# Kernel optimization log

Hardware: AMD Instinct MI355X
Metric: run time of the kernel (lower is better)

Reference implementation:

```python
import jax, jax.numpy as jnp
import numpy as np


def setup_inputs() -> dict:
    key = jax.random.key(0)
    ks = jax.random.split(key, 6)
    B, N, Cd, Qd, E, G = 256, 196, 2048, 1024, 1024, 8
    s = lambda d: 1.0 / np.sqrt(d)
    return {
        "context": jax.random.normal(ks[0], (B, N, Cd), dtype=jnp.float32),
        "query": jax.random.normal(ks[1], (B, Qd), dtype=jnp.float32),
        "Wq": jax.random.normal(ks[2], (E, Qd), dtype=jnp.float32) * s(Qd),
        "bq": jnp.zeros((E,), dtype=jnp.float32),
        "Wc": jax.random.normal(ks[3], (E, Cd), dtype=jnp.float32) * s(Cd),
        "bc": jnp.zeros((E,), dtype=jnp.float32),
        "Wo": jax.random.normal(ks[4], (G, E), dtype=jnp.float32) * s(E),
        "bo": jnp.zeros((G,), dtype=jnp.float32),
    }


def reference(context, query, Wq, bq, Wc, bc, Wo, bo):
    # query: [B, Qd] -> [B, 1, E]; context: [B, N, Cd] -> [B, N, E]
    qp = (query @ Wq.T + bq)[:, None, :]
    cp = jnp.einsum('bnc,ec->bne', context, Wc) + bc
    # dropout in eval mode (identity)
    combined = jnp.tanh(qp + cp)                      # [B, N, E]
    attn = jnp.einsum('bne,ge->bng', combined, Wo) + bo  # [B, N, G]
    weights = jax.nn.softmax(attn, axis=1)            # softmax over regions
    glimpses = jnp.einsum('bng,bnc->bgc', weights, context)  # [B, G, Cd]
    return glimpses.reshape(context.shape[0], -1)     # [B, G*Cd]
```

## Files before the change

kernel.cpp:

```cpp
#include <hip/hip_runtime.h>
#include <stdint.h>

typedef unsigned int u32;
typedef __bf16 bf16_t;
typedef bf16_t bf16x8 __attribute__((ext_vector_type(8)));
typedef bf16_t bf16x4 __attribute__((ext_vector_type(4)));
typedef float  f32x4  __attribute__((ext_vector_type(4)));

#define NB   256
#define NN   196
#define CD   2048
#define QD   1024
#define NE   1024
#define NG   8

#define WS_QP    0
#define WS_ATTN  (NB*NE*4)
#define WS_WCB   (WS_ATTN + NB*NG*NN*4)
#define WS_CTXB  (WS_WCB + (size_t)NE*CD*2)
#define WS_NEED  (WS_CTXB + (size_t)NB*NN*CD*2)

__device__ __forceinline__ bf16_t f2bf(float f){
  u32 u = __float_as_uint(f);
  u += 0x7fffu + ((u >> 16) & 1u);
  unsigned short h = (unsigned short)(u >> 16);
  return __builtin_bit_cast(bf16_t, h);
}

__device__ __forceinline__ float fast_tanh(float x){
  float e = __expf(2.0f * x);
  return 1.0f - 2.0f / (e + 1.0f);
}

__device__ __forceinline__ void load_lds16(const void* g, void* l){
  __builtin_amdgcn_global_load_lds(
      (const __attribute__((address_space(1))) void*)g,
      (__attribute__((address_space(3))) void*)l, 16, 0, 0);
}

__global__ __launch_bounds__(256)
void k_conv(const float* __restrict__ src, bf16_t* __restrict__ dst){
  size_t i = ((size_t)blockIdx.x * 256 + threadIdx.x) * 4;
  float4 v = *(const float4*)(src + i);
  bf16x4 o = { f2bf(v.x), f2bf(v.y), f2bf(v.z), f2bf(v.w) };
  *(bf16x4*)(dst + i) = o;
}

__global__ __launch_bounds__(256)
void k_convctx(const float* __restrict__ src, bf16_t* __restrict__ dst){
  size_t i = ((size_t)blockIdx.x * 256 + threadIdx.x) * 8;
  float4 a = *(const float4*)(src + i);
  float4 b = *(const float4*)(src + i + 4);
  bf16x8 o = { f2bf(a.x), f2bf(a.y), f2bf(a.z), f2bf(a.w),
               f2bf(b.x), f2bf(b.y), f2bf(b.z), f2bf(b.w) };
  *(bf16x8*)(dst + i) = o;
}

__global__ __launch_bounds__(256)
void k_qp(const float* __restrict__ query, const float* __restrict__ Wq,
          const float* __restrict__ bq, float* __restrict__ qp){
  __shared__ float qs[32][36];
  __shared__ float wsm[32][36];
  const u32 t  = threadIdx.x;
  const u32 e0 = blockIdx.x * 32, b0 = blockIdx.y * 32;
  const u32 r  = t >> 3, ci = (t & 7) * 4;
  const u32 tm = (t >> 4) * 2, tn = (t & 15) * 2;
  float c00 = 0.f, c01 = 0.f, c10 = 0.f, c11 = 0.f;
  for (u32 k0 = 0; k0 < QD; k0 += 32){
    float4 qv = *(const float4*)(query + (size_t)(b0 + r) * QD + k0 + ci);
    float4 wv = *(const float4*)(Wq    + (size_t)(e0 + r) * QD + k0 + ci);
    __syncthreads();
    *(float4*)&qs[r][ci]  = qv;
    *(float4*)&wsm[r][ci] = wv;
    __syncthreads();
    #pragma unroll
    for (int kq = 0; kq < 8; kq++){
      float4 a0 = *(const float4*)&qs[tm][kq*4];
      float4 a1 = *(const float4*)&qs[tm+1][kq*4];
      float4 b0v = *(const float4*)&wsm[tn][kq*4];
      float4 b1v = *(const float4*)&wsm[tn+1][kq*4];
      c00 += a0.x*b0v.x + a0.y*b0v.y + a0.z*b0v.z + a0.w*b0v.w;
      c01 += a0.x*b1v.x + a0.y*b1v.y + a0.z*b1v.z + a0.w*b1v.w;
      c10 += a1.x*b0v.x + a1.y*b0v.y + a1.z*b0v.z + a1.w*b0v.w;
      c11 += a1.x*b1v.x + a1.y*b1v.y + a1.z*b1v.z + a1.w*b1v.w;
    }
  }
  float bq0 = bq[e0+tn], bq1 = bq[e0+tn+1];
  qp[(size_t)(b0+tm  )*NE + e0+tn  ] = c00 + bq0;
  qp[(size_t)(b0+tm  )*NE + e0+tn+1] = c01 + bq1;
  qp[(size_t)(b0+tm+1)*NE + e0+tn  ] = c10 + bq0;
  qp[(size_t)(b0+tm+1)*NE + e0+tn+1] = c11 + bq1;
}

#define NKT 32

__global__ __launch_bounds__(512, 2)
void k_main8(const bf16_t* __restrict__ ctxb, const bf16_t* __restrict__ wcb,
             const float* __restrict__ qp, const float* __restrict__ bcv,
             const float* __restrict__ Wo, float* __restrict__ attn)
{
  __shared__ char smem[135168] __attribute__((aligned(128)));

  const u32 tid  = threadIdx.x;
  const u32 lane = tid & 63;
  const u32 w    = tid >> 6;
  const u32 q    = lane >> 4;
  const u32 r15  = lane & 15;
  const u32 x7   = r15 & 7;

  u32 d  = blockIdx.x;
  u32 wg = (d & 7) * 98u + (d >> 3);
  const u32 ms = wg >> 2;
  const u32 ec = wg & 3;
  const u32 m0 = ms * 256;
  const u32 e0 = ec * 256;

  const u32 srow = w*8 + (lane>>3);
  const u32 scol = ((lane&7) ^ ((lane>>3)&7)) * 8;
  const u32 sdst = w*1024u + lane*16u;

  const u32 arow = (w>>1)*32 + r15;
  const u32 brow = (w&1)*64 + r15;

  f32x4 acc[2][2][8];
  #pragma unroll
  for (int a1 = 0; a1 < 2; a1++)
    #pragma unroll
    for (int a2 = 0; a2 < 2; a2++)
      #pragma unroll
      for (int a3 = 0; a3 < 8; a3++) acc[a1][a2][a3] = (f32x4){0.f,0.f,0.f,0.f};

  auto stage = [&](u32 H){
    u32 tile = H >> 2;
    u32 half = H & 3;
    u32 kt   = tile < NKT ? tile : (NKT - 1);
    u32 buf  = tile & 1;
    u32 isb  = half >> 1;
    u32 hh   = half & 1;
    const bf16_t* src = (isb ? (wcb + (size_t)e0 * CD) : (ctxb + (size_t)m0 * CD))
                        + (size_t)(hh*128u + srow) * CD + kt*64u + scol;
    char* dst = smem + buf*65536u + isb*32768u + hh*16384u + sdst;
    load_lds16(src,                  dst);
    load_lds16(src + (size_t)64*CD,  dst + 8192);
  };

  stage(0); stage(1); stage(2); stage(3); stage(4);
  asm volatile("s_waitcnt vmcnt(4)" ::: "memory");
  __builtin_amdgcn_s_barrier();

#define PHASE(QM, QN, HOFF, DOVM) do {                                          \
    const char* Ab_ = smem + bufc*65536u;                                        \
    const char* Bb_ = Ab_ + 32768u;                                              \
    bf16x8 af[2][2], bq_[4][2];                                                  \
    _Pragma("unroll")                                                            \
    for (int m2 = 0; m2 < 2; m2++)                                               \
      _Pragma("unroll")                                                          \
      for (int kk = 0; kk < 2; kk++)                                             \
        af[m2][kk] = *(const bf16x8*)(Ab_ + ((QM)*128u + arow + m2*16u)*128u     \
                                          + (((u32)(kk*4) + q) ^ x7)*16u);       \
    _Pragma("unroll")                                                            \
    for (int nt = 0; nt < 4; nt++)                                               \
      _Pragma("unroll")                                                          \
      for (int kk = 0; kk < 2; kk++)                                             \
        bq_[nt][kk] = *(const bf16x8*)(Bb_ + ((QN)*128u + brow + nt*16u)*128u    \
                                           + (((u32)(kk*4) + q) ^ x7)*16u);      \
    stage(hbase + (HOFF));                                                       \
    __builtin_amdgcn_s_barrier();                                                \
    __builtin_amdgcn_s_setprio(1);                                               \
    _Pragma("unroll")                                                            \
    for (int m2 = 0; m2 < 2; m2++)                                               \
      _Pragma("unroll")                                                          \
      for (int nt = 0; nt < 4; nt++)                                             \
        _Pragma("unroll")                                                        \
        for (int kk = 0; kk < 2; kk++)                                           \
          acc[QM][QN][m2*4+nt] = __builtin_amdgcn_mfma_f32_16x16x32_bf16(        \
              af[m2][kk], bq_[nt][kk], acc[QM][QN][m2*4+nt], 0, 0, 0);           \
    __builtin_amdgcn_s_setprio(0);                                               \
    if (DOVM) asm volatile("s_waitcnt vmcnt(4)" ::: "memory");                   \
    __builtin_amdgcn_s_barrier();                                                \
  } while (0)

  for (u32 kt = 0; kt < NKT; kt++){
    const u32 bufc  = kt & 1;
    const u32 hbase = 4*kt + 5;
    PHASE(0, 0, 0, 1);
    PHASE(0, 1, 1, 0);
    PHASE(1, 0, 2, 0);
    PHASE(1, 1, 3, 1);
  }
#undef PHASE

  asm volatile("s_waitcnt vmcnt(0)" ::: "memory");
  __syncthreads();

  float*  qps  = (float*)(smem + 131072);
  float*  bcs  = (float*)(smem + 134144);
  const u32 b0   = m0 / 196u;
  const u32 bnd1 = (b0 + 1) * 196u - m0;
  const u32 bnd2 = bnd1 + 196u;

  for (u32 idx = tid; idx < 768; idx += 512){
    u32 bb = b0 + idx / 256u;
    if (bb > NB - 1) bb = NB - 1;
    qps[idx] = qp[(size_t)bb * NE + e0 + (idx & 255u)];
  }
  if (tid < 256) bcs[tid] = bcv[e0 + tid];

  bf16x8 wf[8];
  {
    u32 g = r15;
    #pragma unroll
    for (int kk = 0; kk < 8; kk++){
      #pragma unroll
      for (int rr = 0; rr < 8; rr++){
        u32 ei = e0 + kk*32 + q*8 + rr;
        float v = (g < NG) ? Wo[(size_t)g * NE + ei] : 0.0f;
        wf[kk][rr] = f2bf(v);
      }
    }
  }
  __syncthreads();

  #pragma unroll
  for (int qm = 0; qm < 2; qm++)
    #pragma unroll
    for (int qn = 0; qn < 2; qn++)
      #pragma unroll
      for (int t = 0; t < 8; t++){
        u32 rowb = qm*128u + (w>>1)*32u + (t>>2)*16u + q*4u;
        u32 col  = qn*128u + (w&1)*64u + (t&3)*16u + r15;
        float qb = bcs[col];
        #pragma unroll
        for (int r = 0; r < 4; r++){
          u32 row = rowb + r;
          u32 bidx = (row >= bnd1 ? 1u : 0u) + (row >= bnd2 ? 1u : 0u);
          float v = fast_tanh(acc[qm][qn][t][r] + qps[bidx*256u + col] + qb);
          u32 phys = (col >> 3) ^ (row & 7);
          *(bf16_t*)(smem + row*512u + phys*16u + (col&7)*2u) = f2bf(v);
        }
      }
  __syncthreads();

  #pragma unroll
  for (int i = 0; i < 2; i++){
    u32 nrow = w*32u + i*16u + r15;
    f32x4 at = (f32x4){0.f,0.f,0.f,0.f};
    #pragma unroll
    for (int kk = 0; kk < 8; kk++){
      u32 phys = ((u32)(kk*4) + q) ^ (nrow & 7);
      bf16x8 cf = *(const bf16x8*)(smem + nrow*512u + phys*16u);
      at = __builtin_amdgcn_mfma_f32_16x16x32_bf16(wf[kk], cf, at, 0, 0, 0);
    }
    if (q < 2){
      u32 mrow = m0 + nrow;
      u32 bb = mrow / 196u;
      u32 nn = mrow - bb * 196u;
      #pragma unroll
      for (int r = 0; r < 4; r++){
        u32 g = q*4 + r;
        atomicAdd(&attn[((size_t)bb * NG + g) * NN + nn], at[r]);
      }
    }
  }
}

#define BM 128
#define BN 128
#define BK 32
#define KSTEPS (CD/BK)

__global__ __launch_bounds__(256, 2)
void k_main_slow(const float* __restrict__ ctx, const bf16_t* __restrict__ wcb,
                 const float* __restrict__ qp, const float* __restrict__ bcv,
                 const float* __restrict__ Wo, float* __restrict__ attn)
{
  __shared__ char smem[40960] __attribute__((aligned(16)));
  const u32 tid  = threadIdx.x;
  const u32 lane = tid & 63;
  const u32 wave = tid >> 6;
  const u32 wm   = wave >> 1;
  const u32 wn   = wave & 1;
  u32 d  = blockIdx.x;
  u32 x  = d & 7;
  u32 s  = d >> 3;
  u32 ec = s & 7;
  u32 j  = s >> 3;
  u32 ms = j * 8 + x;
  const u32 m0 = ms * BM;
  const u32 e0 = ec * BN;
  const u32 ar  = tid >> 3;
  const u32 ac  = (tid & 7) * 4;
  const u32 br  = tid >> 2;
  const u32 bc8 = (tid & 3) * 8;
  const float*  actx = ctx + (size_t)m0 * CD;
  const bf16_t* bwc  = wcb + (size_t)e0 * CD;
  float4 av[4];
  uint4  bv[2];
  f32x4 acc[4][4];
  #pragma unroll
  for (int i = 0; i < 4; i++)
    #pragma unroll
    for (int jn = 0; jn < 4; jn++) acc[i][jn] = (f32x4){0.f,0.f,0.f,0.f};
  auto issue = [&](u32 ks){
    const u32 k0 = ks * BK;
    #pragma unroll
    for (int p = 0; p < 4; p++)
      av[p] = *(const float4*)(actx + (size_t)(ar + p*32) * CD + k0 + ac);
    #pragma unroll
    for (int p = 0; p < 2; p++)
      bv[p] = *(const uint4*)(bwc + (size_t)(br + p*64) * CD + k0 + bc8);
  };
  auto writebuf = [&](u32 buf){
    bf16_t* A  = (bf16_t*)(smem + buf * 10240u);
    bf16_t* Bb = (bf16_t*)(smem + 20480u + buf * 10240u);
    #pragma unroll
    for (int p = 0; p < 4; p++){
      bf16x4 o = { f2bf(av[p].x), f2bf(av[p].y), f2bf(av[p].z), f2bf(av[p].w) };
      *(bf16x4*)&A[(ar + p*32)*40 + ac] = o;
    }
    #pragma unroll
    for (int p = 0; p < 2; p++)
      *(uint4*)&Bb[(br + p*64)*40 + bc8] = bv[p];
  };
  auto compute = [&](u32 buf){
    bf16_t* A  = (bf16_t*)(smem + buf * 10240u);
    bf16_t* Bb = (bf16_t*)(smem + 20480u + buf * 10240u);
    const u32 kb = (lane >> 4) * 8;
    const u32 rm = wm*64 + (lane & 15);
    const u32 rn = wn*64 + (lane & 15);
    bf16x8 af[4], bfr[4];
    #pragma unroll
    for (int mt = 0; mt < 4; mt++) af[mt]  = *(const bf16x8*)&A[(rm + mt*16)*40 + kb];
    #pragma unroll
    for (int nt = 0; nt < 4; nt++) bfr[nt] = *(const bf16x8*)&Bb[(rn + nt*16)*40 + kb];
    #pragma unroll
    for (int mt = 0; mt < 4; mt++)
      #pragma unroll
      for (int nt = 0; nt < 4; nt++)
        acc[mt][nt] = __builtin_amdgcn_mfma_f32_16x16x32_bf16(af[mt], bfr[nt], acc[mt][nt], 0, 0, 0);
  };
  issue(0); writebuf(0);
  __syncthreads();
  for (u32 ks = 0; ks < KSTEPS; ks++){
    if (ks + 1 < KSTEPS) issue(ks + 1);
    compute(ks & 1);
    __syncthreads();
    if (ks + 1 < KSTEPS){
      writebuf((ks + 1) & 1);
      __syncthreads();
    }
  }
  float*  qp0  = (float*)(smem + 35840);
  float*  qp1  = (float*)(smem + 36352);
  float*  bcs  = (float*)(smem + 36864);
  bf16_t* comb = (bf16_t*)smem;
  const u32 b0  = m0 / 196u;
  const u32 bnd = (b0 + 1) * 196u - m0;
  if (tid < 128){
    qp0[tid] = qp[(size_t)b0 * NE + e0 + tid];
    bcs[tid] = bcv[e0 + tid];
  } else {
    u32 b1 = b0 + 1; if (b1 >= NB) b1 = NB - 1;
    qp1[tid - 128] = qp[(size_t)b1 * NE + e0 + (tid - 128)];
  }
  bf16x8 wf[4];
  {
    u32 g = lane & 15;
    #pragma unroll
    for (int kk = 0; kk < 4; kk++){
      #pragma unroll
      for (int rr = 0; rr < 8; rr++){
        u32 ei = e0 + kk*32 + (lane >> 4)*8 + rr;
        float v = (g < NG) ? Wo[(size_t)g * NE + ei] : 0.0f;
        wf[kk][rr] = f2bf(v);
      }
    }
  }
  __syncthreads();
  #pragma unroll
  for (int nt = 0; nt < 4; nt++){
    u32 el = wn*64 + nt*16 + (lane & 15);
    float qa = qp0[el];
    float qb = qp1[el];
    float bcx = bcs[el];
    #pragma unroll
    for (int mt = 0; mt < 4; mt++){
      u32 rl = wm*64 + mt*16 + (lane >> 4)*4;
      #pragma unroll
      for (int r = 0; r < 4; r++){
        u32 row = rl + r;
        float qv = (row >= bnd) ? qb : qa;
        float t = fast_tanh(acc[mt][nt][r] + qv + bcx);
        comb[row*136 + el] = f2bf(t);
      }
    }
  }
  __syncthreads();
  #pragma unroll
  for (int i = 0; i < 2; i++){
    u32 nrow = (wave*2 + i)*16 + (lane & 15);
    f32x4 at = (f32x4){0.f,0.f,0.f,0.f};
    #pragma unroll
    for (int kk = 0; kk < 4; kk++){
      bf16x8 cf = *(const bf16x8*)&comb[nrow*136 + kk*32 + (lane >> 4)*8];
      at = __builtin_amdgcn_mfma_f32_16x16x32_bf16(wf[kk], cf, at, 0, 0, 0);
    }
    if ((lane >> 4) < 2){
      u32 mrow = m0 + nrow;
      u32 bb = mrow / 196u;
      u32 nn = mrow - bb * 196u;
      #pragma unroll
      for (int r = 0; r < 4; r++){
        u32 g = (lane >> 4)*4 + r;
        atomicAdd(&attn[((size_t)bb * NG + g) * NN + nn], at[r]);
      }
    }
  }
}

__global__ __launch_bounds__(256)
void k_softmax(float* __restrict__ attn){
  u32 flat = blockIdx.x * 4 + (threadIdx.x >> 6);
  u32 lane = threadIdx.x & 63;
  float* row = attn + (size_t)flat * NN;
  float v0 = row[lane];
  float v1 = row[lane + 64];
  float v2 = row[lane + 128];
  float v3 = (lane < 4) ? row[lane + 192] : -1e30f;
  float m = fmaxf(fmaxf(v0, v1), fmaxf(v2, v3));
  #pragma unroll
  for (int o = 1; o < 64; o <<= 1) m = fmaxf(m, __shfl_xor(m, o));
  float e0 = __expf(v0 - m), e1 = __expf(v1 - m), e2 = __expf(v2 - m);
  float e3 = (lane < 4) ? __expf(v3 - m) : 0.f;
  float sum = e0 + e1 + e2 + e3;
  #pragma unroll
  for (int o = 1; o < 64; o <<= 1) sum += __shfl_xor(sum, o);
  float inv = 1.0f / sum;
  row[lane]       = e0 * inv;
  row[lane + 64]  = e1 * inv;
  row[lane + 128] = e2 * inv;
  if (lane < 4) row[lane + 192] = e3 * inv;
}

__global__ __launch_bounds__(256)
void k_glimpse(const float* __restrict__ ctx, const float* __restrict__ w,
               float* __restrict__ out){
  const u32 b  = blockIdx.y;
  const u32 c0 = blockIdx.x * 512 + threadIdx.x * 2;
  __shared__ float ws_[NG * NN];
  for (u32 i = threadIdx.x; i < NG * NN; i += 256)
    ws_[i] = w[(size_t)b * NG * NN + i];
  __syncthreads();
  const float* cp = ctx + (size_t)b * NN * CD + c0;
  float2 acc[NG];
  #pragma unroll
  for (int g = 0; g < NG; g++) acc[g] = make_float2(0.f, 0.f);
  for (u32 n = 0; n < NN; n++){
    float2 v = *(const float2*)(cp + (size_t)n * CD);
    #pragma unroll
    for (int g = 0; g < NG; g++){
      float wv = ws_[g * NN + n];
      acc[g].x = fmaf(wv, v.x, acc[g].x);
      acc[g].y = fmaf(wv, v.y, acc[g].y);
    }
  }
  #pragma unroll
  for (int g = 0; g < NG; g++)
    *(float2*)(out + (size_t)b * (NG * CD) + (size_t)g * CD + c0) = acc[g];
}

extern "C" void kernel_launch(void* const* d_in, const int* in_sizes, int n_in,
                              void* d_out, int out_size, void* d_ws, size_t ws_size,
                              hipStream_t stream)
{
  const float* ctx   = (const float*)d_in[0];
  const float* query = (const float*)d_in[1];
  const float* Wq    = (const float*)d_in[2];
  const float* bq    = (const float*)d_in[3];
  const float* Wc    = (const float*)d_in[4];
  const float* bc    = (const float*)d_in[5];
  const float* Wo    = (const float*)d_in[6];

  char* ws = (char*)d_ws;
  float*  qp   = (float*)(ws + WS_QP);
  float*  attn = (float*)(ws + WS_ATTN);
  bf16_t* wcb  = (bf16_t*)(ws + WS_WCB);
  bf16_t* ctxb = (bf16_t*)(ws + WS_CTXB);
  float*  out  = (float*)d_out;

  (void)hipMemsetAsync(attn, 0, (size_t)NB * NG * NN * 4, stream);
  k_conv<<<2048, 256, 0, stream>>>(Wc, wcb);
  k_qp<<<dim3(32, 8), 256, 0, stream>>>(query, Wq, bq, qp);

  if (ws_size >= (size_t)WS_NEED){
    k_convctx<<<50176, 256, 0, stream>>>(ctx, ctxb);
    k_main8<<<784, 512, 0, stream>>>(ctxb, wcb, qp, bc, Wo, attn);
  } else {
    k_main_slow<<<3136, 256, 0, stream>>>(ctx, wcb, qp, bc, Wo, attn);
  }

  k_softmax<<<512, 256, 0, stream>>>(attn);
  k_glimpse<<<dim3(4, 256), 256, 0, stream>>>(ctx, attn, out);
}
```

Measured before the change: 534.7 us.

## Reuse LDS fragments across quadrant phases and reorder global staging

Reorders the four quadrant MFMA phases into a snake order (00,10,11,01), so each phase reloads only the A or the B fragments from LDS instead of both. This cuts LDS read traffic per k-tile. Global-to-LDS staging now uses precomputed base pointers with a one-tile lookahead, replacing the per-call index arithmetic and the five-stage prologue, and the vmcnt gating points are moved to match. The trade-off is a shallower prefetch distance and a changed wait/barrier pattern, which could expose more global latency or risk ordering hazards on the LDS buffers.

```diff
diff --git a/kernel.cpp b/kernel.cpp
--- a/kernel.cpp
+++ b/kernel.cpp
@@ -122,6 +122,11 @@
   const u32 arow = (w>>1)*32 + r15;
   const u32 brow = (w&1)*64 + r15;
 
+  const bf16_t* pA0 = ctxb + (size_t)(m0 + srow) * CD + scol;
+  const bf16_t* pA1 = pA0 + (size_t)128 * CD;
+  const bf16_t* pB0 = wcb  + (size_t)(e0 + srow) * CD + scol;
+  const bf16_t* pB1 = pB0 + (size_t)128 * CD;
+
   f32x4 acc[2][2][8];
   #pragma unroll
   for (int a1 = 0; a1 < 2; a1++)
@@ -130,65 +135,81 @@
       #pragma unroll
       for (int a3 = 0; a3 < 8; a3++) acc[a1][a2][a3] = (f32x4){0.f,0.f,0.f,0.f};
 
-  auto stage = [&](u32 H){
-    u32 tile = H >> 2;
-    u32 half = H & 3;
-    u32 kt   = tile < NKT ? tile : (NKT - 1);
-    u32 buf  = tile & 1;
-    u32 isb  = half >> 1;
-    u32 hh   = half & 1;
-    const bf16_t* src = (isb ? (wcb + (size_t)e0 * CD) : (ctxb + (size_t)m0 * CD))
-                        + (size_t)(hh*128u + srow) * CD + kt*64u + scol;
-    char* dst = smem + buf*65536u + isb*32768u + hh*16384u + sdst;
-    load_lds16(src,                  dst);
-    load_lds16(src + (size_t)64*CD,  dst + 8192);
+  auto stage = [&](const bf16_t* src, u32 dstoff){
+    load_lds16(src,                 smem + dstoff);
+    load_lds16(src + (size_t)64*CD, smem + dstoff + 8192);
   };
 
-  stage(0); stage(1); stage(2); stage(3); stage(4);
+  stage(pA0, 0u     + sdst);
+  stage(pB0, 32768u + sdst);
+  stage(pA1, 16384u + sdst);
+  stage(pB1, 49152u + sdst);
   asm volatile("s_waitcnt vmcnt(4)" ::: "memory");
   __builtin_amdgcn_s_barrier();
 
-#define PHASE(QM, QN, HOFF, DOVM) do {                                          \
-    const char* Ab_ = smem + bufc*65536u;                                        \
-    const char* Bb_ = Ab_ + 32768u;                                              \
-    bf16x8 af[2][2], bq_[4][2];                                                  \
-    _Pragma("unroll")                                                            \
-    for (int m2 = 0; m2 < 2; m2++)                                               \
-      _Pragma("unroll")                                                          \
-      for (int kk = 0; kk < 2; kk++)                                             \
-        af[m2][kk] = *(const bf16x8*)(Ab_ + ((QM)*128u + arow + m2*16u)*128u     \
-                                          + (((u32)(kk*4) + q) ^ x7)*16u);       \
-    _Pragma("unroll")                                                            \
-    for (int nt = 0; nt < 4; nt++)                                               \
-      _Pragma("unroll")                                                          \
-      for (int kk = 0; kk < 2; kk++)                                             \
-        bq_[nt][kk] = *(const bf16x8*)(Bb_ + ((QN)*128u + brow + nt*16u)*128u    \
-                                           + (((u32)(kk*4) + q) ^ x7)*16u);      \
-    stage(hbase + (HOFF));                                                       \
-    __builtin_amdgcn_s_barrier();                                                \
-    __builtin_amdgcn_s_setprio(1);                                               \
-    _Pragma("unroll")                                                            \
-    for (int m2 = 0; m2 < 2; m2++)                                               \
-      _Pragma("unroll")                                                          \
-      for (int nt = 0; nt < 4; nt++)                                             \
-        _Pragma("unroll")                                                        \
-        for (int kk = 0; kk < 2; kk++)                                           \
-          acc[QM][QN][m2*4+nt] = __builtin_amdgcn_mfma_f32_16x16x32_bf16(        \
-              af[m2][kk], bq_[nt][kk], acc[QM][QN][m2*4+nt], 0, 0, 0);           \
-    __builtin_amdgcn_s_setprio(0);                                               \
-    if (DOVM) asm volatile("s_waitcnt vmcnt(4)" ::: "memory");                   \
-    __builtin_amdgcn_s_barrier();                                                \
-  } while (0)
+  bf16x8 afr[2][2], bfr[4][2];
+
+#define LOAD_A(QM) do{                                                          \
+    _Pragma("unroll")                                                           \
+    for (int m2 = 0; m2 < 2; m2++)                                              \
+      _Pragma("unroll")                                                         \
+      for (int kk = 0; kk < 2; kk++)                                            \
+        afr[m2][kk] = *(const bf16x8*)(Ab_ + ((QM)*128u + arow + m2*16u)*128u   \
+                                           + (((u32)(kk*4) + q) ^ x7)*16u);     \
+  }while(0)
+
+#define LOAD_B(QN) do{                                                          \
+    _Pragma("unroll")                                                           \
+    for (int nt = 0; nt < 4; nt++)                                              \
+      _Pragma("unroll")                                                         \
+      for (int kk = 0; kk < 2; kk++)                                            \
+        bfr[nt][kk] = *(const bf16x8*)(Bb_ + ((QN)*128u + brow + nt*16u)*128u   \
+                                           + (((u32)(kk*4) + q) ^ x7)*16u);     \
+  }while(0)
+
+#define MFMA16(QM, QN) do{                                                      \
+    __builtin_amdgcn_s_setprio(1);                                              \
+    _Pragma("unroll")                                                           \
+    for (int m2 = 0; m2 < 2; m2++)                                              \
+      _Pragma("unroll")                                                         \
+      for (int nt = 0; nt < 4; nt++)                                            \
+        _Pragma("unroll")                                                       \
+        for (int kk = 0; kk < 2; kk++)                                          \
+          acc[QM][QN][m2*4+nt] = __builtin_amdgcn_mfma_f32_16x16x32_bf16(       \
+              afr[m2][kk], bfr[nt][kk], acc[QM][QN][m2*4+nt], 0, 0, 0);         \
+    __builtin_amdgcn_s_setprio(0);                                              \
+  }while(0)
+
+#define VMGATE asm volatile("s_waitcnt vmcnt(4)" ::: "memory")
+#define BAR    __builtin_amdgcn_s_barrier()
 
   for (u32 kt = 0; kt < NKT; kt++){
-    const u32 bufc  = kt & 1;
-    const u32 hbase = 4*kt + 5;
-    PHASE(0, 0, 0, 1);
-    PHASE(0, 1, 1, 0);
-    PHASE(1, 0, 2, 0);
-    PHASE(1, 1, 3, 1);
-  }
-#undef PHASE
+    const char* Ab_ = smem + (kt & 1) * 65536u;
+    const char* Bb_ = Ab_ + 32768u;
+    const u32 kn = ((kt + 1 < NKT) ? (kt + 1) : (NKT - 1)) * 64u;
+    const u32 bo = ((kt + 1) & 1) * 65536u + sdst;
+
+    LOAD_A(0); LOAD_B(0);
+    stage(pA0 + kn, bo + 0u);
+    BAR;  MFMA16(0,0);  VMGATE;  BAR;
+
+    LOAD_A(1);
+    stage(pB0 + kn, bo + 32768u);
+    BAR;  MFMA16(1,0);  VMGATE;  BAR;
+
+    LOAD_B(1);
+    stage(pA1 + kn, bo + 16384u);
+    BAR;  MFMA16(1,1);  BAR;
+
+    LOAD_A(0);
+    stage(pB1 + kn, bo + 49152u);
+    BAR;  MFMA16(0,1);  VMGATE;  BAR;
+  }
+#undef LOAD_A
+#undef LOAD_B
+#undef MFMA16
+#undef VMGATE
+#undef BAR
 
   asm volatile("s_waitcnt vmcnt(0)" ::: "memory");
   __syncthreads();
```

Measured after the change: 507.9 us. 5.0% less time.
